# Kernel optimization log

Measured on AMD Instinct MI355X. Metric: run time of the kernel, lower is better.

## Reference

```python
import jax, jax.numpy as jnp
import numpy as np

N = 100000
E = 3200000
HID = 256
C = 10
T = 12
D = 8
HEADS = 4
LH = HID // 2  # LSTM hidden = hidden_dim // 2


def setup_inputs() -> dict:
    key = jax.random.key(0)
    ks = jax.random.split(key, 16)
    rn = lambda k, shp, s=0.05: jax.random.normal(k, shp, dtype=jnp.float32) * s
    return {
        "embeddings": jax.random.normal(ks[0], (N, HID), dtype=jnp.float32),
        "predictions": jax.random.normal(ks[1], (N, C), dtype=jnp.float32),
        "temporal_features": jax.random.normal(ks[2], (N, T, D), dtype=jnp.float32),
        "edge_index": jax.random.randint(ks[3], (2, E), 0, N),
        "cW1": rn(ks[4], (HID // 2, HID)), "cb1": jnp.zeros((HID // 2,), jnp.float32),
        "cW2": rn(ks[5], (1, HID // 2)), "cb2": jnp.zeros((1,), jnp.float32),
        "w_ih0": rn(ks[6], (4 * LH, C)), "w_hh0": rn(ks[7], (4 * LH, LH)),
        "b_ih0": jnp.zeros((4 * LH,), jnp.float32), "b_hh0": jnp.zeros((4 * LH,), jnp.float32),
        "w_ih1": rn(ks[8], (4 * LH, LH)), "w_hh1": rn(ks[9], (4 * LH, LH)),
        "b_ih1": jnp.zeros((4 * LH,), jnp.float32), "b_hh1": jnp.zeros((4 * LH,), jnp.float32),
        "gW": rn(ks[10], (C, HEADS * C)), "ga_src": rn(ks[11], (HEADS, C)),
        "ga_dst": rn(ks[12], (HEADS, C)), "gb": jnp.zeros((C,), jnp.float32),
    }


def _lstm_layer(x, w_ih, w_hh, b_ih, b_hh):
    # x: [N, T, I]; PyTorch gate order i, f, g, o
    n = x.shape[0]
    h_dim = w_hh.shape[1]
    def step(carry, xt):
        h, c = carry
        g = xt @ w_ih.T + h @ w_hh.T + b_ih + b_hh  # [N, 4H]
        i, f, gg, o = jnp.split(g, 4, axis=-1)
        c = jax.nn.sigmoid(f) * c + jax.nn.sigmoid(i) * jnp.tanh(gg)
        h = jax.nn.sigmoid(o) * jnp.tanh(c)
        return (h, c), h
    init = (jnp.zeros((n, h_dim), x.dtype), jnp.zeros((n, h_dim), x.dtype))
    _, hs = jax.lax.scan(step, init, jnp.swapaxes(x, 0, 1))  # [T, N, H]
    return jnp.swapaxes(hs, 0, 1)


def _gat(probs, src, dst, gW, ga_src, ga_dst, gb, n):
    x = (probs @ gW).reshape(n, HEADS, C)  # [N, H, C]
    a_s = (x * ga_src).sum(-1)  # [N, H]
    a_d = (x * ga_dst).sum(-1)
    e = jax.nn.leaky_relu(a_s[src] + a_d[dst], 0.2)  # [E, H]
    m = jax.ops.segment_max(e, dst, num_segments=n)
    ex = jnp.exp(e - m[dst])
    s = jax.ops.segment_sum(ex, dst, num_segments=n)
    alpha = ex / (s[dst] + 1e-16)  # edge softmax per destination
    out = jax.ops.segment_sum(alpha[:, :, None] * x[src], dst, num_segments=n)
    return out.mean(axis=1) + gb  # concat=False -> head mean, plus bias


def reference(embeddings, predictions, temporal_features, edge_index,
              cW1, cb1, cW2, cb2,
              w_ih0, w_hh0, b_ih0, b_hh0, w_ih1, w_hh1, b_ih1, b_hh1,
              gW, ga_src, ga_dst, gb):
    n = predictions.shape[0]
    probs = jax.nn.softmax(predictions, axis=-1)
    max_probs = probs.max(axis=-1)
    pseudo_labels = jnp.argmax(probs, axis=-1)

    # confidence_net (dropout inactive in eval)
    h = jax.nn.relu(embeddings @ cW1.T + cb1)
    embedding_confidence = jax.nn.sigmoid(h @ cW2.T + cb2)[:, 0]

    # temporal consistency: same prediction repeated T times through 2-layer LSTM
    t = temporal_features.shape[1]
    pred_seq = jnp.broadcast_to(predictions[:, None, :], (n, t, predictions.shape[1]))
    l1 = _lstm_layer(pred_seq, w_ih0, w_hh0, b_ih0, b_hh0)
    l2 = _lstm_layer(l1, w_ih1, w_hh1, b_ih1, b_hh1)
    temporal_variance = jnp.var(l2, axis=1, ddof=1).mean(axis=-1)  # torch.var unbiased
    temporal_confidence = 1.0 / (1.0 + temporal_variance)

    # self-loops (used by both GATConv and agreement check)
    loops = jnp.arange(n, dtype=edge_index.dtype)
    src = jnp.concatenate([edge_index[0], loops])
    dst = jnp.concatenate([edge_index[1], loops])

    gout = _gat(probs, src, dst, gW, ga_src, ga_dst, gb, n)
    num = (probs * gout).sum(-1)
    den = jnp.maximum(jnp.linalg.norm(probs, axis=-1) * jnp.linalg.norm(gout, axis=-1), 1e-8)
    graph_confidence = ((num / den) + 1.0) / 2.0

    combined = (0.4 * max_probs + 0.2 * embedding_confidence
                + 0.2 * temporal_confidence + 0.2 * graph_confidence)
    confident_mask = combined > 0.85

    # neighborhood agreement via segment-sum scatter (replaces per-edge loop)
    deg = jax.ops.segment_sum(jnp.ones_like(src, jnp.float32), src, num_segments=n)
    oh = jax.nn.one_hot(pseudo_labels, C, dtype=jnp.float32)
    nsum = jax.ops.segment_sum(oh[src], dst, num_segments=n)
    navg = nsum / (deg[:, None] + 1e-8)
    agreement = jnp.take_along_axis(navg, pseudo_labels[:, None], axis=1)[:, 0] >= 0.6
    final_mask = confident_mask & agreement

    entropy = -(probs * jnp.log(probs + 1e-8)).sum(-1)
    uncertainty = entropy / np.log(C).astype(np.float32)

    return (pseudo_labels, combined, final_mask, max_probs,
            embedding_confidence, temporal_confidence, graph_confidence, uncertainty)
```

## Files before the change

kernel.cpp:

```cpp
#include <hip/hip_runtime.h>
#include <hip/hip_bf16.h>


#define HIDN 256
#define NC 10
#define TSTEPS 12
#define NHEADS 4
#define LH 128

typedef __attribute__((ext_vector_type(8))) short short8;
typedef __attribute__((ext_vector_type(4))) float floatx4;

__device__ __forceinline__ unsigned short f2bf(float x) {
  unsigned u = __float_as_uint(x);
  u = u + 0x7FFFu + ((u >> 16) & 1u);
  return (unsigned short)(u >> 16);
}
__device__ __forceinline__ unsigned char f2fp8(float x) {
  return (unsigned char)(__builtin_amdgcn_cvt_pk_fp8_f32(x, 0.f, 0, false) & 0xff);
}
__device__ __forceinline__ float fexp2(float x) { return __builtin_amdgcn_exp2f(x); }
__device__ __forceinline__ float frcpf(float x) { return __builtin_amdgcn_rcpf(x); }
#define LOG2E 1.44269504f
__device__ __forceinline__ float sigf(float x) {
  return frcpf(1.0f + fexp2(-LOG2E * x));
}
__device__ __forceinline__ float sig2(float x) {
  return frcpf(1.f + fexp2(-LOG2E * x));
}
__device__ __forceinline__ float tanh2(float x) {
  return 1.f - 2.f * frcpf(1.f + fexp2((2.f * LOG2E) * x));
}
__device__ __forceinline__ floatx4 mfma16(short8 a, short8 b, floatx4 c) {
  return __builtin_amdgcn_mfma_f32_16x16x32_bf16(a, b, c, 0, 0, 0);
}
__device__ __forceinline__ floatx4 mfma8(long a, long b, floatx4 c) {
  return __builtin_amdgcn_mfma_f32_16x16x32_fp8_fp8(a, b, c, 0, 0, 0);
}

__global__ __launch_bounds__(256) void probs_kernel(
    const float* __restrict__ pred, const float* __restrict__ gW,
    const float* __restrict__ gas, const float* __restrict__ gad,
    float* __restrict__ out, float* __restrict__ wp16,
    float* __restrict__ wad, float* __restrict__ wmp, int N) {
  __shared__ float sgW[400], sgas[40], sgad[40];
  int tid = threadIdx.x;
  for (int i = tid; i < 400; i += 256) sgW[i] = gW[i];
  if (tid < 40) { sgas[tid] = gas[tid]; sgad[tid] = gad[tid]; }
  __syncthreads();
  int node = blockIdx.x * 256 + tid;
  if (node >= N) return;
  const float* pr = pred + (size_t)node * NC;
  float p[NC];
#pragma unroll
  for (int c = 0; c < NC; c++) p[c] = pr[c];
  float pm = p[0]; int arg = 0;
#pragma unroll
  for (int c = 1; c < NC; c++) if (p[c] > pm) { pm = p[c]; arg = c; }
  float s = 0.f, prb[NC];
#pragma unroll
  for (int c = 0; c < NC; c++) { prb[c] = __expf(p[c] - pm); s += prb[c]; }
  float inv = 1.f / s;
  float ent = 0.f;
#pragma unroll
  for (int c = 0; c < NC; c++) {
    prb[c] *= inv;
    ent -= prb[c] * __logf(prb[c] + 1e-8f);
  }
  out[node] = (float)arg;
  out[(size_t)3 * N + node] = inv;
  out[(size_t)7 * N + node] = ent * (1.f / 2.302585093f);
  wmp[node] = inv;
  float xv[40];
#pragma unroll
  for (int hc = 0; hc < 40; hc++) {
    float t = 0.f;
#pragma unroll
    for (int k = 0; k < NC; k++) t += prb[k] * sgW[k * 40 + hc];
    xv[hc] = t;
  }
  float asv[4];
#pragma unroll
  for (int h = 0; h < NHEADS; h++) {
    float as = 0.f, ad = 0.f;
#pragma unroll
    for (int c = 0; c < NC; c++) { as += xv[h * 10 + c] * sgas[h * 10 + c]; ad += xv[h * 10 + c] * sgad[h * 10 + c]; }
    asv[h] = as;
    wad[(size_t)node * 4 + h] = ad;
  }
  float4* wp = (float4*)(wp16 + (size_t)node * 16);
  wp[0] = make_float4(prb[0], prb[1], prb[2], prb[3]);
  wp[1] = make_float4(prb[4], prb[5], prb[6], prb[7]);
  wp[2] = make_float4(prb[8], prb[9], asv[0], asv[1]);
  wp[3] = make_float4(asv[2], asv[3], __int_as_float(arg), 0.f);
}

__global__ __launch_bounds__(256) void pack_kernel(
    const float* __restrict__ whh0, const float* __restrict__ wih0,
    const float* __restrict__ wih1, const float* __restrict__ whh1,
    const float* __restrict__ cw1,
    unsigned char* __restrict__ PB1, unsigned char* __restrict__ PB2,
    unsigned short* __restrict__ PBc) {
  int idx = blockIdx.x * 256 + threadIdx.x;
  if (idx < 81920) {
    int j = idx & 7, lane = (idx >> 3) & 63, rest = idx >> 9;
    int g = rest & 3, w = (rest >> 2) & 7, ks = rest >> 5;
    int k = ks * 32 + ((lane >> 4) << 3) + j;
    int u = w * 16 + (lane & 15), row = g * 128 + u;
    float val = 0.f;
    if (k < 128) val = whh0[row * 128 + k];
    else if (k < 138) val = wih0[row * 10 + (k - 128)];
    PB1[idx] = f2fp8(val);
  }
  if (idx < 131072) {
    int j = idx & 7, lane = (idx >> 3) & 63, rest = idx >> 9;
    int g = rest & 3, w = (rest >> 2) & 7, ks = rest >> 5;
    int k = ks * 32 + ((lane >> 4) << 3) + j;
    int u = w * 16 + (lane & 15), row = g * 128 + u;
    float val = (k < 128) ? wih1[row * 128 + k] : whh1[row * 128 + (k - 128)];
    PB2[idx] = f2fp8(val);
  }
  if (idx < 32768) {
    int j = idx & 7, lane = (idx >> 3) & 63, t2 = idx >> 9;
    int ti = t2 & 7, ks = t2 >> 3;
    int n = ti * 16 + (lane & 15);
    int k = ks * 32 + ((lane >> 4) << 3) + j;
    PBc[idx] = f2bf(cw1[n * 256 + k]);
  }
}

__global__ void rankhist_kernel(const int* __restrict__ ei, int* __restrict__ shin,
                                int* __restrict__ shout, int* __restrict__ erank,
                                int E, int N) {
  int idx = blockIdx.x * 256 + threadIdx.x;
  if (idx >= E + N) return;
  int sh = blockIdx.x & 7;
  int src, dst;
  if (idx < E) { src = ei[idx]; dst = ei[E + idx]; } else { src = dst = idx - E; }
  int r = atomicAdd(&shin[(size_t)sh * N + dst], 1);
  atomicAdd(&shout[(size_t)sh * N + src], 1);
  erank[idx] = r;
}

__global__ __launch_bounds__(256) void conf_kernel(
    const float* __restrict__ emb, const unsigned short* __restrict__ PBc,
    const float* __restrict__ cb1, const float* __restrict__ cw2,
    const float* __restrict__ cb2, float* __restrict__ wec, int N) {
  __shared__ __align__(16) unsigned short astage[128 * 264];
  int tid = threadIdx.x;
  int base = blockIdx.x * 128;
  for (int i = tid * 4; i < 128 * 256; i += 1024) {
    int row = i >> 8, col = i & 255;
    float4 v = make_float4(0.f, 0.f, 0.f, 0.f);
    if (base + row < N) v = *(const float4*)(emb + (size_t)(base + row) * 256 + col);
    unsigned short* d = &astage[row * 264 + col];
    d[0] = f2bf(v.x); d[1] = f2bf(v.y); d[2] = f2bf(v.z); d[3] = f2bf(v.w);
  }
  __syncthreads();
  int wave = tid >> 6, lane = tid & 63, quad = lane >> 4, ln = lane & 15;
  float b1f[8], w2f[8];
#pragma unroll
  for (int t = 0; t < 8; t++) { b1f[t] = cb1[t * 16 + ln]; w2f[t] = cw2[t * 16 + ln]; }
  floatx4 acc[2][8];
#pragma unroll
  for (int mi = 0; mi < 2; mi++)
#pragma unroll
    for (int t = 0; t < 8; t++) acc[mi][t] = (floatx4){b1f[t], b1f[t], b1f[t], b1f[t]};
#pragma unroll
  for (int ks = 0; ks < 8; ks++) {
    short8 a0 = *(const short8*)&astage[(wave * 32 + ln) * 264 + ks * 32 + quad * 8];
    short8 a1 = *(const short8*)&astage[(wave * 32 + 16 + ln) * 264 + ks * 32 + quad * 8];
    const unsigned short* bp = PBc + (((size_t)(ks * 8) * 64 + lane) << 3);
#pragma unroll
    for (int t = 0; t < 8; t++) {
      short8 b = *(const short8*)(bp + (size_t)t * 512);
      acc[0][t] = mfma16(a0, b, acc[0][t]);
      acc[1][t] = mfma16(a1, b, acc[1][t]);
    }
  }
  float part[2][4];
#pragma unroll
  for (int mi = 0; mi < 2; mi++)
#pragma unroll
    for (int r = 0; r < 4; r++) {
      float t = 0.f;
#pragma unroll
      for (int ti = 0; ti < 8; ti++) t += fmaxf(acc[mi][ti][r], 0.f) * w2f[ti];
      part[mi][r] = t;
    }
#pragma unroll
  for (int off = 8; off >= 1; off >>= 1)
#pragma unroll
    for (int mi = 0; mi < 2; mi++)
#pragma unroll
      for (int r = 0; r < 4; r++) part[mi][r] += __shfl_xor(part[mi][r], off);
  if (ln == 0) {
    float b2 = cb2[0];
#pragma unroll
    for (int mi = 0; mi < 2; mi++)
#pragma unroll
      for (int r = 0; r < 4; r++) {
        int node = base + wave * 32 + mi * 16 + quad * 4 + r;
        if (node < N) wec[node] = sigf(part[mi][r] + b2);
      }
  }
}

__global__ __launch_bounds__(256) void scan1_kernel(
    const int* __restrict__ shin, const int* __restrict__ shout,
    int* __restrict__ shbase, int* __restrict__ outdeg,
    int* __restrict__ rowptr, int* __restrict__ partials, int N) {
  int t = threadIdx.x, b = blockIdx.x;
  int base = b * 1024 + t * 4;
  int tot[4];
#pragma unroll
  for (int j = 0; j < 4; j++) {
    int i = base + j;
    int run = 0;
    if (i < N) {
      int od = 0;
#pragma unroll
      for (int sh = 0; sh < 8; sh++) {
        int v = shin[(size_t)sh * N + i];
        shbase[(size_t)sh * N + i] = run;
        run += v;
        od += shout[(size_t)sh * N + i];
      }
      outdeg[i] = od;
    }
    tot[j] = run;
  }
  int tsum = tot[0] + tot[1] + tot[2] + tot[3];
  int lane = t & 63, wv = t >> 6;
  int x = tsum;
#pragma unroll
  for (int d = 1; d < 64; d <<= 1) { int y = __shfl_up(x, d); if (lane >= d) x += y; }
  __shared__ int wsum[4];
  if (lane == 63) wsum[wv] = x;
  __syncthreads();
  int wo = 0;
  for (int i = 0; i < wv; i++) wo += wsum[i];
  int excl = wo + x - tsum;
  if (base + 0 < N) rowptr[base + 0] = excl;
  if (base + 1 < N) rowptr[base + 1] = excl + tot[0];
  if (base + 2 < N) rowptr[base + 2] = excl + tot[0] + tot[1];
  if (base + 3 < N) rowptr[base + 3] = excl + tot[0] + tot[1] + tot[2];
  if (t == 255) partials[b] = wo + x;
}

__global__ void scan2_kernel(int* __restrict__ partials, int nb) {
  int t = threadIdx.x;
  int lane = t & 63, wv = t >> 6;
  int v = (t < nb) ? partials[t] : 0;
  int x = v;
#pragma unroll
  for (int d = 1; d < 64; d <<= 1) { int y = __shfl_up(x, d); if (lane >= d) x += y; }
  __shared__ int wsum[4];
  if (lane == 63) wsum[wv] = x;
  __syncthreads();
  int wo = 0;
  for (int i = 0; i < wv; i++) wo += wsum[i];
  if (t < nb) partials[t] = wo + x - v;
}

__global__ void scan3_kernel(int* __restrict__ rowptr, int* __restrict__ shbase,
                             const int* __restrict__ partials, int N, int total) {
  int i = blockIdx.x * 256 + threadIdx.x;
  if (i < N) {
    int r = rowptr[i] + partials[i >> 10];
    rowptr[i] = r;
#pragma unroll
    for (int sh = 0; sh < 8; sh++) shbase[(size_t)sh * N + i] += r;
  }
  if (i == 0) rowptr[N] = total;
}

__global__ void scatterrank_kernel(const int* __restrict__ ei,
                                   const int* __restrict__ shbase,
                                   const int* __restrict__ erank,
                                   int* __restrict__ csr, int E, int N) {
  int idx = blockIdx.x * 256 + threadIdx.x;
  if (idx >= E + N) return;
  int sh = (idx >> 8) & 7;
  int src, dst;
  if (idx < E) { src = ei[idx]; dst = ei[E + idx]; } else { src = dst = idx - E; }
  csr[shbase[(size_t)sh * N + dst] + erank[idx]] = src;
}

__global__ __launch_bounds__(256) void gather_kernel(
    const int* __restrict__ rowptr, const int* __restrict__ csr,
    const float* __restrict__ wp16, const float* __restrict__ wad,
    const int* __restrict__ outdeg, const float* __restrict__ gW,
    const float* __restrict__ gb, float* __restrict__ wgc,
    float* __restrict__ wag, int N) {
  __shared__ float sgW[400];
  int tid = threadIdx.x;
  for (int i = tid; i < 400; i += 256) sgW[i] = gW[i];
  __syncthreads();
  int vgid = blockIdx.x * 256 + tid;
  int node = vgid >> 2, par = vgid & 3;
  if (node >= N) return;
  int beg = rowptr[node], end = rowptr[node + 1];
  float4 ad4 = *(const float4*)(wad + (size_t)node * 4);
  const float4* myrec = (const float4*)(wp16 + (size_t)node * 16);
  float4 m3 = myrec[3];
  int mylab = __float_as_int(m3.z);
  float ssum0 = 0.f, ssum1 = 0.f, ssum2 = 0.f, ssum3 = 0.f, cnt = 0.f;
  float z[4][10];
#pragma unroll
  for (int h = 0; h < 4; h++)
#pragma unroll
    for (int c = 0; c < 10; c++) z[h][c] = 0.f;
  for (int e = beg + par; e < end; e += 4) {
    int s = csr[e];
    const float4* rp = (const float4*)(wp16 + (size_t)s * 16);
    float4 r0 = rp[0], r1 = rp[1], r2 = rp[2], r3 = rp[3];
    float p[10] = {r0.x, r0.y, r0.z, r0.w, r1.x, r1.y, r1.z, r1.w, r2.x, r2.y};
    float as[4] = {r2.z, r2.w, r3.x, r3.y};
    float adh[4] = {ad4.x, ad4.y, ad4.z, ad4.w};
    cnt += (__float_as_int(r3.z) == mylab) ? 1.f : 0.f;
#pragma unroll
    for (int h = 0; h < 4; h++) {
      float v = as[h] + adh[h];
      float lr = v >= 0.f ? v : 0.2f * v;
      float ex = fexp2(LOG2E * lr);
      if (h == 0) ssum0 += ex; else if (h == 1) ssum1 += ex;
      else if (h == 2) ssum2 += ex; else ssum3 += ex;
#pragma unroll
      for (int c = 0; c < 10; c++) z[h][c] += ex * p[c];
    }
  }
#pragma unroll
  for (int mask = 1; mask <= 2; mask <<= 1) {
    cnt += __shfl_xor(cnt, mask);
    ssum0 += __shfl_xor(ssum0, mask); ssum1 += __shfl_xor(ssum1, mask);
    ssum2 += __shfl_xor(ssum2, mask); ssum3 += __shfl_xor(ssum3, mask);
#pragma unroll
    for (int h = 0; h < 4; h++)
#pragma unroll
      for (int c = 0; c < 10; c++) z[h][c] += __shfl_xor(z[h][c], mask);
  }
  float zp[10], sp;
  if (par == 0) { sp = ssum0;
#pragma unroll
    for (int c = 0; c < 10; c++) zp[c] = z[0][c];
  } else if (par == 1) { sp = ssum1;
#pragma unroll
    for (int c = 0; c < 10; c++) zp[c] = z[1][c];
  } else if (par == 2) { sp = ssum2;
#pragma unroll
    for (int c = 0; c < 10; c++) zp[c] = z[2][c];
  } else { sp = ssum3;
#pragma unroll
    for (int c = 0; c < 10; c++) zp[c] = z[3][c];
  }
  float inv = 1.f / (sp + 1e-16f);
  float gpart[10];
#pragma unroll
  for (int c = 0; c < 10; c++) {
    float t = 0.f;
#pragma unroll
    for (int k = 0; k < 10; k++) t += zp[k] * sgW[k * 40 + par * 10 + c];
    gpart[c] = t * inv;
  }
#pragma unroll
  for (int c = 0; c < 10; c++) {
    gpart[c] += __shfl_xor(gpart[c], 1);
    gpart[c] += __shfl_xor(gpart[c], 2);
  }
  if (par == 0) {
    float4 m0 = myrec[0], m1 = myrec[1], m2 = myrec[2];
    float pn[10] = {m0.x, m0.y, m0.z, m0.w, m1.x, m1.y, m1.z, m1.w, m2.x, m2.y};
    float num = 0.f, np2 = 0.f, ng2 = 0.f;
#pragma unroll
    for (int c = 0; c < 10; c++) {
      float g = gpart[c] * 0.25f + gb[c];
      float p = pn[c];
      num += p * g;
      np2 += p * p;
      ng2 += g * g;
    }
    float den = fmaxf(sqrtf(np2) * sqrtf(ng2), 1e-8f);
    wgc[node] = (num / den + 1.f) * 0.5f;
    float dgv = (float)outdeg[node];
    wag[node] = cnt / (dgv + 1e-8f);
  }
}

#define HB2 4352

__global__ __launch_bounds__(512, 2) void lstm_kernel(
    const float* __restrict__ pred, const unsigned char* __restrict__ PB1,
    const unsigned char* __restrict__ PB2,
    const float* __restrict__ bih0, const float* __restrict__ bhh0,
    const float* __restrict__ bih1, const float* __restrict__ bhh1,
    const float* __restrict__ wmp, const float* __restrict__ wec,
    const float* __restrict__ wgc, const float* __restrict__ wag,
    float* __restrict__ out, int N) {
  __shared__ __align__(16) unsigned char hb[4 * HB2];
  __shared__ __align__(16) unsigned char xbuf[32 * 40];
  __shared__ float varsum[32];
  int tid = threadIdx.x;
  int base = blockIdx.x * 32;
  for (int i = tid * 4; i < HB2; i += 2048) *(int*)&hb[3 * HB2 + i] = 0;
  for (int i = tid; i < 32 * 40; i += 512) {
    int nd = i / 40, o = i - nd * 40;
    float v = 0.f;
    if (o < 10 && base + nd < N) v = pred[(size_t)(base + nd) * NC + o];
    xbuf[i] = f2fp8(v);
  }
  if (tid < 32) varsum[tid] = 0.f;
  int wave = tid >> 6, lane = tid & 63, quad = lane >> 4, ln = lane & 15;
  float b0f[4], b1f[4];
#pragma unroll
  for (int g = 0; g < 4; g++) {
    int row = g * 128 + wave * 16 + ln;
    b0f[g] = bih0[row] + bhh0[row];
    b1f[g] = bih1[row] + bhh1[row];
  }
  long w1r[5][4], w2r[8][4];
#pragma unroll
  for (int ks = 0; ks < 5; ks++)
#pragma unroll
    for (int g = 0; g < 4; g++)
      w1r[ks][g] = *(const long*)(PB1 + (size_t)(((ks * 8 + wave) * 4 + g) * 64 + lane) * 8);
#pragma unroll
  for (int ks = 0; ks < 8; ks++)
#pragma unroll
    for (int g = 0; g < 4; g++)
      w2r[ks][g] = *(const long*)(PB2 + (size_t)(((ks * 8 + wave) * 4 + g) * 64 + lane) * 8);
  float c1[8], c2[8], s1[8], s2[8];
#pragma unroll
  for (int i = 0; i < 8; i++) { c1[i] = 0.f; c2[i] = 0.f; s1[i] = 0.f; s2[i] = 0.f; }
  const int hq = quad * 8;
  const int ucol = wave * 16 + ln;
  int arow[2], wrow[2];
#pragma unroll
  for (int mt = 0; mt < 2; mt++) {
    arow[mt] = (mt * 16 + ln) * 136 + hq;
    wrow[mt] = (mt * 16 + quad * 4) * 136 + ucol;
  }
  __syncthreads();
  long xa[2];
  xa[0] = *(const long*)&xbuf[ln * 40 + hq];
  xa[1] = *(const long*)&xbuf[(16 + ln) * 40 + hq];

  {
    floatx4 acc[2][4];
#pragma unroll
    for (int mt = 0; mt < 2; mt++)
#pragma unroll
      for (int g = 0; g < 4; g++) acc[mt][g] = (floatx4){b0f[g], b0f[g], b0f[g], b0f[g]};
#pragma unroll
    for (int g = 0; g < 4; g++)
#pragma unroll
      for (int mt = 0; mt < 2; mt++) acc[mt][g] = mfma8(xa[mt], w1r[4][g], acc[mt][g]);
#pragma unroll
    for (int mt = 0; mt < 2; mt++)
#pragma unroll
      for (int r = 0; r < 4; r++) {
        int ci = mt * 4 + r;
        float ig = sig2(acc[mt][0][r]);
        float gg = tanh2(acc[mt][2][r]);
        float og = sig2(acc[mt][3][r]);
        float c = ig * gg;
        c1[ci] = c;
        hb[0 + wrow[mt] + r * 136] = f2fp8(og * tanh2(c));
      }
  }

#define LSTM_SEG(O1R, O1W, O2R, O2W, lastseg)                                    \
  {                                                                              \
    __syncthreads();                                                             \
    floatx4 acc[2][4];                                                           \
    _Pragma("unroll") for (int mt = 0; mt < 2; mt++)                             \
        _Pragma("unroll") for (int g = 0; g < 4; g++)                            \
            acc[mt][g] = (floatx4){b1f[g], b1f[g], b1f[g], b1f[g]};              \
    _Pragma("unroll") for (int ks = 0; ks < 8; ks++) {                           \
      long a_[2];                                                                \
      if (ks < 4) {                                                              \
        _Pragma("unroll") for (int mt = 0; mt < 2; mt++)                         \
            a_[mt] = *(const long*)&hb[(O1R) + arow[mt] + ks * 32];              \
      } else {                                                                   \
        _Pragma("unroll") for (int mt = 0; mt < 2; mt++)                         \
            a_[mt] = *(const long*)&hb[(O2R) + arow[mt] + (ks - 4) * 32];        \
      }                                                                          \
      _Pragma("unroll") for (int g = 0; g < 4; g++)                              \
          _Pragma("unroll") for (int mt = 0; mt < 2; mt++)                       \
              acc[mt][g] = mfma8(a_[mt], w2r[ks][g], acc[mt][g]);                \
    }                                                                            \
    _Pragma("unroll") for (int mt = 0; mt < 2; mt++)                             \
        _Pragma("unroll") for (int r = 0; r < 4; r++) {                          \
      int ci = mt * 4 + r;                                                       \
      float ig = sig2(acc[mt][0][r]);                                            \
      float fg = sig2(acc[mt][1][r]);                                            \
      float gg = tanh2(acc[mt][2][r]);                                           \
      float og = sig2(acc[mt][3][r]);                                            \
      float c = fg * c2[ci] + ig * gg;                                           \
      c2[ci] = c;                                                                \
      float h = og * tanh2(c);                                                   \
      s1[ci] += h;                                                               \
      s2[ci] += h * h;                                                           \
      hb[(O2W) + wrow[mt] + r * 136] = f2fp8(h);                                 \
    }                                                                            \
    if (!(lastseg)) {                                                            \
      _Pragma("unroll") for (int mt = 0; mt < 2; mt++)                           \
          _Pragma("unroll") for (int g = 0; g < 4; g++)                          \
              acc[mt][g] = (floatx4){b0f[g], b0f[g], b0f[g], b0f[g]};            \
      _Pragma("unroll") for (int ks = 0; ks < 5; ks++) {                         \
        long a_[2];                                                              \
        if (ks < 4) {                                                            \
          _Pragma("unroll") for (int mt = 0; mt < 2; mt++)                       \
              a_[mt] = *(const long*)&hb[(O1R) + arow[mt] + ks * 32];            \
        } else {                                                                 \
          a_[0] = xa[0]; a_[1] = xa[1];                                          \
        }                                                                        \
        _Pragma("unroll") for (int g = 0; g < 4; g++)                            \
            _Pragma("unroll") for (int mt = 0; mt < 2; mt++)                     \
                acc[mt][g] = mfma8(a_[mt], w1r[ks][g], acc[mt][g]);              \
      }                                                                          \
      _Pragma("unroll") for (int mt = 0; mt < 2; mt++)                           \
          _Pragma("unroll") for (int r = 0; r < 4; r++) {                        \
        int ci = mt * 4 + r;                                                     \
        float ig = sig2(acc[mt][0][r]);                                          \
        float fg = sig2(acc[mt][1][r]);                                          \
        float gg = tanh2(acc[mt][2][r]);                                         \
        float og = sig2(acc[mt][3][r]);                                          \
        float c = fg * c1[ci] + ig * gg;                                         \
        c1[ci] = c;                                                              \
        hb[(O1W) + wrow[mt] + r * 136] = f2fp8(og * tanh2(c));                   \
      }                                                                          \
    }                                                                            \
  }

  for (int tt = 0; tt < TSTEPS / 2; tt++) {
    LSTM_SEG(0, HB2, 3 * HB2, 2 * HB2, false);
    LSTM_SEG(HB2, 0, 2 * HB2, 3 * HB2, tt == TSTEPS / 2 - 1);
  }
#undef LSTM_SEG

#pragma unroll
  for (int mt = 0; mt < 2; mt++)
#pragma unroll
    for (int r = 0; r < 4; r++) {
      int ci = mt * 4 + r;
      float m = s1[ci] * (1.f / 12.f);
      float var = (s2[ci] - 12.f * m * m) * (1.f / 11.f);
      atomicAdd(&varsum[mt * 16 + quad * 4 + r], var);
    }
  __syncthreads();
  if (tid < 32 && base + tid < N) {
    int node = base + tid;
    float tc = 1.f / (1.f + varsum[tid] * (1.f / 128.f));
    float mp = wmp[node], ec = wec[node], gc = wgc[node];
    float comb = 0.4f * mp + 0.2f * ec + 0.2f * tc + 0.2f * gc;
    bool mask = (comb > 0.85f) && (wag[node] >= 0.6f);
    out[(size_t)1 * N + node] = comb;
    out[(size_t)2 * N + node] = mask ? 1.f : 0.f;
    out[(size_t)4 * N + node] = ec;
    out[(size_t)5 * N + node] = tc;
    out[(size_t)6 * N + node] = gc;
  }
}

extern "C" void kernel_launch(void* const* d_in, const int* in_sizes, int n_in,
                              void* d_out, int out_size, void* d_ws, size_t ws_size,
                              hipStream_t stream) {
  const float* emb  = (const float*)d_in[0];
  const float* pred = (const float*)d_in[1];
  const int*   ei   = (const int*)d_in[3];
  const float* cw1  = (const float*)d_in[4];
  const float* cb1  = (const float*)d_in[5];
  const float* cw2  = (const float*)d_in[6];
  const float* cb2  = (const float*)d_in[7];
  const float* wih0 = (const float*)d_in[8];
  const float* whh0 = (const float*)d_in[9];
  const float* bih0 = (const float*)d_in[10];
  const float* bhh0 = (const float*)d_in[11];
  const float* wih1 = (const float*)d_in[12];
  const float* whh1 = (const float*)d_in[13];
  const float* bih1 = (const float*)d_in[14];
  const float* bhh1 = (const float*)d_in[15];
  const float* gW   = (const float*)d_in[16];
  const float* gas  = (const float*)d_in[17];
  const float* gad  = (const float*)d_in[18];
  const float* gb   = (const float*)d_in[19];

  const int N = in_sizes[0] / HIDN;
  const int E = in_sizes[3] / 2;
  float* out = (float*)d_out;
  float* ws = (float*)d_ws;
  const size_t sN = (size_t)N;
  const size_t sE = (size_t)E;

  float* wp16   = ws;
  float* wad    = ws + 16 * sN;
  float* wmp    = ws + 20 * sN;
  float* wec    = ws + 21 * sN;
  float* wgc    = ws + 22 * sN;
  float* wag    = ws + 23 * sN;
  int* outdeg   = (int*)(ws + 24 * sN);
  int* rowptr   = (int*)(ws + 25 * sN);
  int* shin     = (int*)(ws + 26 * sN) + 64;
  int* shout    = shin + 8 * sN;
  int* shbase   = shout + 8 * sN;
  int* partials = shbase + 8 * sN + 64;
  int* erank    = partials + 256 + 64;
  int* csr      = erank + sE + sN + 64;
  float* pbase  = (float*)(csr + sE + sN + 64);
  unsigned char* PB1 = (unsigned char*)pbase;
  unsigned char* PB2 = (unsigned char*)(pbase + 20480);
  unsigned short* PBc = (unsigned short*)(pbase + 53248);

  hipMemsetAsync(shin, 0, 16 * sN * sizeof(int), stream);

  probs_kernel<<<(N + 255) / 256, 256, 0, stream>>>(
      pred, gW, gas, gad, out, wp16, wad, wmp, N);
  pack_kernel<<<512, 256, 0, stream>>>(whh0, wih0, wih1, whh1, cw1, PB1, PB2, PBc);
  int ne = E + N;
  rankhist_kernel<<<(ne + 255) / 256, 256, 0, stream>>>(ei, shin, shout, erank, E, N);

  conf_kernel<<<(N + 127) / 128, 256, 0, stream>>>(emb, PBc, cb1, cw2, cb2, wec, N);

  int nb = (N + 1023) / 1024;
  scan1_kernel<<<nb, 256, 0, stream>>>(shin, shout, shbase, outdeg, rowptr, partials, N);
  scan2_kernel<<<1, 256, 0, stream>>>(partials, nb);
  scan3_kernel<<<(N + 255) / 256, 256, 0, stream>>>(rowptr, shbase, partials, N, ne);

  scatterrank_kernel<<<(ne + 255) / 256, 256, 0, stream>>>(ei, shbase, erank, csr, E, N);

  gather_kernel<<<(4 * N + 255) / 256, 256, 0, stream>>>(
      rowptr, csr, wp16, wad, outdeg, gW, gb, wgc, wag, N);

  lstm_kernel<<<(N + 31) / 32, 512, 0, stream>>>(
      pred, PB1, PB2, bih0, bhh0, bih1, bhh1, wmp, wec, wgc, wag, out, N);
}
```

Baseline: 1.332 ms.

## Merge independent launches into combined kernels and cut LSTM register pressure for occupancy

Folds probs, pack and rankhist into one launch, and conf and scan1 into a second, dispatching on block index. This removes launch gaps and lets the independent work overlap. scan3 no longer adds the row offsets into all 8 shard bases; scatterrank adds rowptr itself instead. The LSTM kernel now keeps only half of the layer-1 weights in registers, reloads the rest from global memory each step through volatile loads, and reads biases from shared memory, so it can raise launch bounds from 2 to 4 blocks per SM. The catch is extra global and LDS traffic inside the recurrent loop.

```diff
diff --git a/kernel.cpp b/kernel.cpp
--- a/kernel.cpp
+++ b/kernel.cpp
@@ -38,17 +38,17 @@
   return __builtin_amdgcn_mfma_f32_16x16x32_fp8_fp8(a, b, c, 0, 0, 0);
 }
 
-__global__ __launch_bounds__(256) void probs_kernel(
+__device__ __forceinline__ void probs_body(
+    int bb, float* sgW, float* sgas, float* sgad,
     const float* __restrict__ pred, const float* __restrict__ gW,
     const float* __restrict__ gas, const float* __restrict__ gad,
     float* __restrict__ out, float* __restrict__ wp16,
     float* __restrict__ wad, float* __restrict__ wmp, int N) {
-  __shared__ float sgW[400], sgas[40], sgad[40];
   int tid = threadIdx.x;
   for (int i = tid; i < 400; i += 256) sgW[i] = gW[i];
   if (tid < 40) { sgas[tid] = gas[tid]; sgad[tid] = gad[tid]; }
   __syncthreads();
-  int node = blockIdx.x * 256 + tid;
+  int node = bb * 256 + tid;
   if (node >= N) return;
   const float* pr = pred + (size_t)node * NC;
   float p[NC];
@@ -95,13 +95,13 @@
   wp[3] = make_float4(asv[2], asv[3], __int_as_float(arg), 0.f);
 }
 
-__global__ __launch_bounds__(256) void pack_kernel(
-    const float* __restrict__ whh0, const float* __restrict__ wih0,
+__device__ __forceinline__ void pack_body(
+    int bb, const float* __restrict__ whh0, const float* __restrict__ wih0,
     const float* __restrict__ wih1, const float* __restrict__ whh1,
     const float* __restrict__ cw1,
     unsigned char* __restrict__ PB1, unsigned char* __restrict__ PB2,
     unsigned short* __restrict__ PBc) {
-  int idx = blockIdx.x * 256 + threadIdx.x;
+  int idx = bb * 256 + threadIdx.x;
   if (idx < 81920) {
     int j = idx & 7, lane = (idx >> 3) & 63, rest = idx >> 9;
     int g = rest & 3, w = (rest >> 2) & 7, ks = rest >> 5;
@@ -129,12 +129,12 @@
   }
 }
 
-__global__ void rankhist_kernel(const int* __restrict__ ei, int* __restrict__ shin,
-                                int* __restrict__ shout, int* __restrict__ erank,
-                                int E, int N) {
-  int idx = blockIdx.x * 256 + threadIdx.x;
+__device__ __forceinline__ void rankhist_body(
+    int bb, int realblk, const int* __restrict__ ei, int* __restrict__ shin,
+    int* __restrict__ shout, int* __restrict__ erank, int E, int N) {
+  int idx = bb * 256 + threadIdx.x;
   if (idx >= E + N) return;
-  int sh = blockIdx.x & 7;
+  int sh = realblk & 7;
   int src, dst;
   if (idx < E) { src = ei[idx]; dst = ei[E + idx]; } else { src = dst = idx - E; }
   int r = atomicAdd(&shin[(size_t)sh * N + dst], 1);
@@ -142,13 +142,36 @@
   erank[idx] = r;
 }
 
-__global__ __launch_bounds__(256) void conf_kernel(
+__global__ __launch_bounds__(256) void mega1_kernel(
+    const float* __restrict__ pred, const float* __restrict__ gW,
+    const float* __restrict__ gas, const float* __restrict__ gad,
+    float* __restrict__ out, float* __restrict__ wp16,
+    float* __restrict__ wad, float* __restrict__ wmp,
+    const float* __restrict__ whh0, const float* __restrict__ wih0,
+    const float* __restrict__ wih1, const float* __restrict__ whh1,
+    const float* __restrict__ cw1,
+    unsigned char* __restrict__ PB1, unsigned char* __restrict__ PB2,
+    unsigned short* __restrict__ PBc,
+    const int* __restrict__ ei, int* __restrict__ shin, int* __restrict__ shout,
+    int* __restrict__ erank, int N, int E, int GP, int GK) {
+  __shared__ float sgW[400], sgas[40], sgad[40];
+  int b = blockIdx.x;
+  if (b < GP) {
+    probs_body(b, sgW, sgas, sgad, pred, gW, gas, gad, out, wp16, wad, wmp, N);
+  } else if (b < GP + GK) {
+    pack_body(b - GP, whh0, wih0, wih1, whh1, cw1, PB1, PB2, PBc);
+  } else {
+    rankhist_body(b - GP - GK, b, ei, shin, shout, erank, E, N);
+  }
+}
+
+__device__ __forceinline__ void conf_body(
+    int bb, unsigned short* astage,
     const float* __restrict__ emb, const unsigned short* __restrict__ PBc,
     const float* __restrict__ cb1, const float* __restrict__ cw2,
     const float* __restrict__ cb2, float* __restrict__ wec, int N) {
-  __shared__ __align__(16) unsigned short astage[128 * 264];
   int tid = threadIdx.x;
-  int base = blockIdx.x * 128;
+  int base = bb * 128;
   for (int i = tid * 4; i < 128 * 256; i += 1024) {
     int row = i >> 8, col = i & 255;
     float4 v = make_float4(0.f, 0.f, 0.f, 0.f);
@@ -206,12 +229,12 @@
   }
 }
 
-__global__ __launch_bounds__(256) void scan1_kernel(
-    const int* __restrict__ shin, const int* __restrict__ shout,
+__device__ __forceinline__ void scan1_body(
+    int bb, int* wsum, const int* __restrict__ shin, const int* __restrict__ shout,
     int* __restrict__ shbase, int* __restrict__ outdeg,
     int* __restrict__ rowptr, int* __restrict__ partials, int N) {
-  int t = threadIdx.x, b = blockIdx.x;
-  int base = b * 1024 + t * 4;
+  int t = threadIdx.x;
+  int base = bb * 1024 + t * 4;
   int tot[4];
 #pragma unroll
   for (int j = 0; j < 4; j++) {
@@ -235,7 +258,6 @@
   int x = tsum;
 #pragma unroll
   for (int d = 1; d < 64; d <<= 1) { int y = __shfl_up(x, d); if (lane >= d) x += y; }
-  __shared__ int wsum[4];
   if (lane == 63) wsum[wv] = x;
   __syncthreads();
   int wo = 0;
@@ -245,7 +267,23 @@
   if (base + 1 < N) rowptr[base + 1] = excl + tot[0];
   if (base + 2 < N) rowptr[base + 2] = excl + tot[0] + tot[1];
   if (base + 3 < N) rowptr[base + 3] = excl + tot[0] + tot[1] + tot[2];
-  if (t == 255) partials[b] = wo + x;
+  if (t == 255) partials[bb] = wo + x;
+}
+
+__global__ __launch_bounds__(256) void mega2_kernel(
+    const float* __restrict__ emb, const unsigned short* __restrict__ PBc,
+    const float* __restrict__ cb1, const float* __restrict__ cw2,
+    const float* __restrict__ cb2, float* __restrict__ wec,
+    const int* __restrict__ shin, const int* __restrict__ shout,
+    int* __restrict__ shbase, int* __restrict__ outdeg,
+    int* __restrict__ rowptr, int* __restrict__ partials, int N, int GC) {
+  __shared__ __align__(16) unsigned short astage[128 * 264];
+  int b = blockIdx.x;
+  if (b < GC) {
+    conf_body(b, astage, emb, PBc, cb1, cw2, cb2, wec, N);
+  } else {
+    scan1_body(b - GC, (int*)astage, shin, shout, shbase, outdeg, rowptr, partials, N);
+  }
 }
 
 __global__ void scan2_kernel(int* __restrict__ partials, int nb) {
@@ -263,28 +301,24 @@
   if (t < nb) partials[t] = wo + x - v;
 }
 
-__global__ void scan3_kernel(int* __restrict__ rowptr, int* __restrict__ shbase,
+__global__ void scan3_kernel(int* __restrict__ rowptr,
                              const int* __restrict__ partials, int N, int total) {
   int i = blockIdx.x * 256 + threadIdx.x;
-  if (i < N) {
-    int r = rowptr[i] + partials[i >> 10];
-    rowptr[i] = r;
-#pragma unroll
-    for (int sh = 0; sh < 8; sh++) shbase[(size_t)sh * N + i] += r;
-  }
+  if (i < N) rowptr[i] = rowptr[i] + partials[i >> 10];
   if (i == 0) rowptr[N] = total;
 }
 
 __global__ void scatterrank_kernel(const int* __restrict__ ei,
+                                   const int* __restrict__ rowptr,
                                    const int* __restrict__ shbase,
                                    const int* __restrict__ erank,
-                                   int* __restrict__ csr, int E, int N) {
+                                   int* __restrict__ csr, int E, int N, int GPK) {
   int idx = blockIdx.x * 256 + threadIdx.x;
   if (idx >= E + N) return;
-  int sh = (idx >> 8) & 7;
+  int sh = (GPK + (idx >> 8)) & 7;
   int src, dst;
   if (idx < E) { src = ei[idx]; dst = ei[E + idx]; } else { src = dst = idx - E; }
-  csr[shbase[(size_t)sh * N + dst] + erank[idx]] = src;
+  csr[rowptr[dst] + shbase[(size_t)sh * N + dst] + erank[idx]] = src;
 }
 
 __global__ __launch_bounds__(256) void gather_kernel(
@@ -389,7 +423,7 @@
 
 #define HB2 4352
 
-__global__ __launch_bounds__(512, 2) void lstm_kernel(
+__global__ __launch_bounds__(512, 4) void lstm_kernel(
     const float* __restrict__ pred, const unsigned char* __restrict__ PB1,
     const unsigned char* __restrict__ PB2,
     const float* __restrict__ bih0, const float* __restrict__ bhh0,
@@ -399,6 +433,7 @@
     float* __restrict__ out, int N) {
   __shared__ __align__(16) unsigned char hb[4 * HB2];
   __shared__ __align__(16) unsigned char xbuf[32 * 40];
+  __shared__ float sbias[1024];
   __shared__ float varsum[32];
   int tid = threadIdx.x;
   int base = blockIdx.x * 32;
@@ -409,23 +444,13 @@
     if (o < 10 && base + nd < N) v = pred[(size_t)(base + nd) * NC + o];
     xbuf[i] = f2fp8(v);
   }
+  sbias[tid] = bih0[tid] + bhh0[tid];
+  sbias[512 + tid] = bih1[tid] + bhh1[tid];
   if (tid < 32) varsum[tid] = 0.f;
   int wave = tid >> 6, lane = tid & 63, quad = lane >> 4, ln = lane & 15;
-  float b0f[4], b1f[4];
-#pragma unroll
-  for (int g = 0; g < 4; g++) {
-    int row = g * 128 + wave * 16 + ln;
-    b0f[g] = bih0[row] + bhh0[row];
-    b1f[g] = bih1[row] + bhh1[row];
-  }
-  long w1r[5][4], w2r[8][4];
-#pragma unroll
-  for (int ks = 0; ks < 5; ks++)
-#pragma unroll
-    for (int g = 0; g < 4; g++)
-      w1r[ks][g] = *(const long*)(PB1 + (size_t)(((ks * 8 + wave) * 4 + g) * 64 + lane) * 8);
-#pragma unroll
-  for (int ks = 0; ks < 8; ks++)
+  long w2r[4][4];
+#pragma unroll
+  for (int ks = 0; ks < 4; ks++)
 #pragma unroll
     for (int g = 0; g < 4; g++)
       w2r[ks][g] = *(const long*)(PB2 + (size_t)(((ks * 8 + wave) * 4 + g) * 64 + lane) * 8);
@@ -441,20 +466,23 @@
     wrow[mt] = (mt * 16 + quad * 4) * 136 + ucol;
   }
   __syncthreads();
-  long xa[2];
-  xa[0] = *(const long*)&xbuf[ln * 40 + hq];
-  xa[1] = *(const long*)&xbuf[(16 + ln) * 40 + hq];
 
   {
+    long xa0 = *(const long*)&xbuf[ln * 40 + hq];
+    long xa1 = *(const long*)&xbuf[(16 + ln) * 40 + hq];
     floatx4 acc[2][4];
 #pragma unroll
-    for (int mt = 0; mt < 2; mt++)
-#pragma unroll
-      for (int g = 0; g < 4; g++) acc[mt][g] = (floatx4){b0f[g], b0f[g], b0f[g], b0f[g]};
-#pragma unroll
-    for (int g = 0; g < 4; g++)
-#pragma unroll
-      for (int mt = 0; mt < 2; mt++) acc[mt][g] = mfma8(xa[mt], w1r[4][g], acc[mt][g]);
+    for (int g = 0; g < 4; g++) {
+      float b0 = sbias[g * 128 + ucol];
+      acc[0][g] = (floatx4){b0, b0, b0, b0};
+      acc[1][g] = (floatx4){b0, b0, b0, b0};
+    }
+#pragma unroll
+    for (int g = 0; g < 4; g++) {
+      long wv = *(const long*)(PB1 + (size_t)(((4 * 8 + wave) * 4 + g) * 64 + lane) * 8);
+      acc[0][g] = mfma8(xa0, wv, acc[0][g]);
+      acc[1][g] = mfma8(xa1, wv, acc[1][g]);
+    }
 #pragma unroll
     for (int mt = 0; mt < 2; mt++)
 #pragma unroll
@@ -473,21 +501,28 @@
   {                                                                              \
     __syncthreads();                                                             \
     floatx4 acc[2][4];                                                           \
-    _Pragma("unroll") for (int mt = 0; mt < 2; mt++)                             \
-        _Pragma("unroll") for (int g = 0; g < 4; g++)                            \
-            acc[mt][g] = (floatx4){b1f[g], b1f[g], b1f[g], b1f[g]};              \
+    _Pragma("unroll") for (int g = 0; g < 4; g++) {                              \
+      float b1 = sbias[512 + g * 128 + ucol];                                    \
+      acc[0][g] = (floatx4){b1, b1, b1, b1};                                     \
+      acc[1][g] = (floatx4){b1, b1, b1, b1};                                     \
+    }                                                                            \
     _Pragma("unroll") for (int ks = 0; ks < 8; ks++) {                           \
-      long a_[2];                                                                \
+      long a0_, a1_;                                                             \
       if (ks < 4) {                                                              \
-        _Pragma("unroll") for (int mt = 0; mt < 2; mt++)                         \
-            a_[mt] = *(const long*)&hb[(O1R) + arow[mt] + ks * 32];              \
+        a0_ = *(const long*)&hb[(O1R) + arow[0] + ks * 32];                      \
+        a1_ = *(const long*)&hb[(O1R) + arow[1] + ks * 32];                      \
       } else {                                                                   \
-        _Pragma("unroll") for (int mt = 0; mt < 2; mt++)                         \
-            a_[mt] = *(const long*)&hb[(O2R) + arow[mt] + (ks - 4) * 32];        \
+        a0_ = *(const long*)&hb[(O2R) + arow[0] + (ks - 4) * 32];                \
+        a1_ = *(const long*)&hb[(O2R) + arow[1] + (ks - 4) * 32];                \
       }                                                                          \
-      _Pragma("unroll") for (int g = 0; g < 4; g++)                              \
-          _Pragma("unroll") for (int mt = 0; mt < 2; mt++)                       \
-              acc[mt][g] = mfma8(a_[mt], w2r[ks][g], acc[mt][g]);                \
+      _Pragma("unroll") for (int g = 0; g < 4; g++) {                            \
+        long wv;                                                                 \
+        if (ks < 4) wv = w2r[ks][g];                                             \
+        else wv = *(volatile const long*)(PB2 +                                  \
+                 (size_t)(((ks * 8 + wave) * 4 + g) * 64 + lane) * 8);           \
+        acc[0][g] = mfma8(a0_, wv, acc[0][g]);                                   \
+        acc[1][g] = mfma8(a1_, wv, acc[1][g]);                                   \
+      }                                                                          \
     }                                                                            \
     _Pragma("unroll") for (int mt = 0; mt < 2; mt++)                             \
         _Pragma("unroll") for (int r = 0; r < 4; r++) {                          \
@@ -504,20 +539,26 @@
       hb[(O2W) + wrow[mt] + r * 136] = f2fp8(h);                                 \
     }                                                                            \
     if (!(lastseg)) {                                                            \
-      _Pragma("unroll") for (int mt = 0; mt < 2; mt++)                           \
-          _Pragma("unroll") for (int g = 0; g < 4; g++)                          \
-              acc[mt][g] = (floatx4){b0f[g], b0f[g], b0f[g], b0f[g]};            \
+      _Pragma("unroll") for (int g = 0; g < 4; g++) {                            \
+        float b0 = sbias[g * 128 + ucol];                                        \
+        acc[0][g] = (floatx4){b0, b0, b0, b0};                                   \
+        acc[1][g] = (floatx4){b0, b0, b0, b0};                                   \
+      }                                                                          \
       _Pragma("unroll") for (int ks = 0; ks < 5; ks++) {                         \
-        long a_[2];                                                              \
+        long a0_, a1_;                                                           \
         if (ks < 4) {                                                            \
-          _Pragma("unroll") for (int mt = 0; mt < 2; mt++)                       \
-              a_[mt] = *(const long*)&hb[(O1R) + arow[mt] + ks * 32];            \
+          a0_ = *(const long*)&hb[(O1R) + arow[0] + ks * 32];                    \
+          a1_ = *(const long*)&hb[(O1R) + arow[1] + ks * 32];                    \
         } else {                                                                 \
-          a_[0] = xa[0]; a_[1] = xa[1];                                          \
+          a0_ = *(const long*)&xbuf[ln * 40 + hq];                               \
+          a1_ = *(const long*)&xbuf[(16 + ln) * 40 + hq];                        \
         }                                                                        \
-        _Pragma("unroll") for (int g = 0; g < 4; g++)                            \
-            _Pragma("unroll") for (int mt = 0; mt < 2; mt++)                     \
-                acc[mt][g] = mfma8(a_[mt], w1r[ks][g], acc[mt][g]);              \
+        _Pragma("unroll") for (int g = 0; g < 4; g++) {                          \
+          long wv = *(volatile const long*)(PB1 +                                \
+                   (size_t)(((ks * 8 + wave) * 4 + g) * 64 + lane) * 8);         \
+          acc[0][g] = mfma8(a0_, wv, acc[0][g]);                                 \
+          acc[1][g] = mfma8(a1_, wv, acc[1][g]);                                 \
+        }                                                                        \
       }                                                                          \
       _Pragma("unroll") for (int mt = 0; mt < 2; mt++)                           \
           _Pragma("unroll") for (int r = 0; r < 4; r++) {                        \
@@ -614,20 +655,25 @@
 
   hipMemsetAsync(shin, 0, 16 * sN * sizeof(int), stream);
 
-  probs_kernel<<<(N + 255) / 256, 256, 0, stream>>>(
-      pred, gW, gas, gad, out, wp16, wad, wmp, N);
-  pack_kernel<<<512, 256, 0, stream>>>(whh0, wih0, wih1, whh1, cw1, PB1, PB2, PBc);
+  int GP = (N + 255) / 256, GK = 512;
   int ne = E + N;
-  rankhist_kernel<<<(ne + 255) / 256, 256, 0, stream>>>(ei, shin, shout, erank, E, N);
-
-  conf_kernel<<<(N + 127) / 128, 256, 0, stream>>>(emb, PBc, cb1, cw2, cb2, wec, N);
-
+  int GH = (ne + 255) / 256;
+  mega1_kernel<<<GP + GK + GH, 256, 0, stream>>>(
+      pred, gW, gas, gad, out, wp16, wad, wmp,
+      whh0, wih0, wih1, whh1, cw1, PB1, PB2, PBc,
+      ei, shin, shout, erank, N, E, GP, GK);
+
+  int GC = (N + 127) / 128;
   int nb = (N + 1023) / 1024;
-  scan1_kernel<<<nb, 256, 0, stream>>>(shin, shout, shbase, outdeg, rowptr, partials, N);
+  mega2_kernel<<<GC + nb, 256, 0, stream>>>(
+      emb, PBc, cb1, cw2, cb2, wec, shin, shout, shbase, outdeg, rowptr,
+      partials, N, GC);
+
   scan2_kernel<<<1, 256, 0, stream>>>(partials, nb);
-  scan3_kernel<<<(N + 255) / 256, 256, 0, stream>>>(rowptr, shbase, partials, N, ne);
-
-  scatterrank_kernel<<<(ne + 255) / 256, 256, 0, stream>>>(ei, shbase, erank, csr, E, N);
+  scan3_kernel<<<(N + 255) / 256, 256, 0, stream>>>(rowptr, partials, N, ne);
+
+  scatterrank_kernel<<<(ne + 255) / 256, 256, 0, stream>>>(
+      ei, rowptr, shbase, erank, csr, E, N, GP + GK);
 
   gather_kernel<<<(4 * N + 255) / 256, 256, 0, stream>>>(
       rowptr, csr, wp16, wad, outdeg, gW, gb, wgc, wag, N);
```

New measurement: 2.600 ms. 95.2% more time.
